# Optimization experiments

Hardware: AMD Instinct MI355X
Metric: run time of the kernel (lower is better)

The kernel has to match this reference:

```python
import jax, jax.numpy as jnp
import numpy as np

B, L, EMBED = 8, 4096, 1024
HEADS, WIN, SHIFT = 16, 128, 64
HD = EMBED // HEADS
MLP_HIDDEN = 4 * EMBED
SCALE = HD ** -0.5
NW = L // WIN


def _layer_norm(x, w, b, eps=1e-5):
    m = x.mean(-1, keepdims=True)
    v = x.var(-1, keepdims=True)
    return (x - m) * jax.lax.rsqrt(v + eps) * w + b


def _compute_mask():
    # replicate SwinBlock1D._compute_mask: region ids over full L, then windowed
    sizes = [L - WIN, WIN - SHIFT, SHIFT]
    region = np.zeros(L, np.int32)
    pos = 0
    for i, s in enumerate(sizes):
        region[pos:pos + s] = i
        pos += s
    region = region.reshape(NW, WIN)
    diff = region[:, None, :] - region[:, :, None]  # (nW, W, W)
    return jnp.asarray(np.where(diff != 0, -100.0, 0.0).astype(np.float32))


_MASK = _compute_mask()
_REL_IDX = jnp.arange(WIN)[None, :] - jnp.arange(WIN)[:, None] + WIN - 1  # (W, W)


def setup_inputs() -> dict:
    key = jax.random.key(0)
    ks = jax.random.split(key, 8)
    s = 0.02

    def w(k, shape):
        return jax.random.normal(k, shape, jnp.float32) * s

    return {
        "x": jax.random.normal(ks[0], (B, L, EMBED), jnp.float32),
        "qkv_w": w(ks[1], (3 * EMBED, EMBED)),
        "qkv_b": jnp.zeros((3 * EMBED,), jnp.float32),
        "proj_w": w(ks[2], (EMBED, EMBED)),
        "proj_b": jnp.zeros((EMBED,), jnp.float32),
        "rpb": w(ks[3], (2 * WIN - 1, HEADS)),
        "norm1_w": jnp.ones((EMBED,), jnp.float32),
        "norm1_b": jnp.zeros((EMBED,), jnp.float32),
        "norm2_w": jnp.ones((EMBED,), jnp.float32),
        "norm2_b": jnp.zeros((EMBED,), jnp.float32),
        "mlp_w1": w(ks[4], (MLP_HIDDEN, EMBED)),
        "mlp_b1": jnp.zeros((MLP_HIDDEN,), jnp.float32),
        "mlp_w2": w(ks[5], (EMBED, MLP_HIDDEN)),
        "mlp_b2": jnp.zeros((EMBED,), jnp.float32),
    }


def reference(x, qkv_w, qkv_b, proj_w, proj_b, rpb,
              norm1_w, norm1_b, norm2_w, norm2_b,
              mlp_w1, mlp_b1, mlp_w2, mlp_b2):
    BW = B * NW
    shortcut = x
    h = _layer_norm(x, norm1_w, norm1_b)
    # shifted-window attention (shift_size > 0)
    h = jnp.roll(h, -SHIFT, axis=1)
    win = h.reshape(BW, WIN, EMBED)
    qkv = (win @ qkv_w.T + qkv_b).reshape(BW, WIN, 3, HEADS, HD)
    qkv = qkv.transpose(2, 0, 3, 1, 4)  # (3, BW, H, W, hd)
    q, k, v = qkv[0], qkv[1], qkv[2]
    attn = jnp.einsum('bhqd,bhkd->bhqk', q, k) * SCALE
    bias = rpb[_REL_IDX]  # (W, W, H)
    attn = attn + bias.transpose(2, 0, 1)[None]
    attn = attn.reshape(B, NW, HEADS, WIN, WIN) + _MASK[None, :, None]
    attn = jax.nn.softmax(attn.reshape(BW, HEADS, WIN, WIN), axis=-1)
    # dropout layers are identity in eval mode
    out = jnp.einsum('bhqk,bhkd->bhqd', attn, v)
    out = out.transpose(0, 2, 1, 3).reshape(BW, WIN, EMBED)
    out = out @ proj_w.T + proj_b
    out = out.reshape(B, L, EMBED)
    out = jnp.roll(out, SHIFT, axis=1)
    x = shortcut + out
    # MLP block
    h2 = _layer_norm(x, norm2_w, norm2_b)
    h2 = jax.nn.gelu(h2 @ mlp_w1.T + mlp_b1, approximate=False) @ mlp_w2.T + mlp_b2
    return x + h2
```

## Files before the change

kernel.cpp:

```cpp
#include <hip/hip_runtime.h>
#include <cstdint>
#include <cstddef>

#define SEQ_L   4096
#define EMBED   1024
#define HEADS   16
#define WINSZ   128
#define SHIFTSZ 64
#define HD      64
#define NWIN    32
#define MTOT    32768
#define ATT_SCALE 0.125f

typedef __bf16 bf16x8 __attribute__((ext_vector_type(8)));
typedef float  f32x4  __attribute__((ext_vector_type(4)));

typedef __attribute__((address_space(3))) void       lds_void;
typedef const __attribute__((address_space(1))) void gbl_void;

#define GLDS16(g, s) __builtin_amdgcn_global_load_lds((gbl_void*)(g), (lds_void*)(s), 16, 0, 0)

__device__ __forceinline__ unsigned short f2bf(float f) {
    unsigned int u = __float_as_uint(f);
    u += 0x7fffu + ((u >> 16) & 1u);
    return (unsigned short)(u >> 16);
}

__launch_bounds__(256)
__global__ void wconv4(const float* __restrict__ s0, const float* __restrict__ s1,
                       const float* __restrict__ s2, const float* __restrict__ s3,
                       unsigned short* __restrict__ d0, unsigned short* __restrict__ d1,
                       unsigned short* __restrict__ d2, unsigned short* __restrict__ d3)
{
    const int b = blockIdx.x;
    const float* s; unsigned short* d; int off;
    if (b < 3072)      { s = s0; d = d0; off = b; }
    else if (b < 4096) { s = s1; d = d1; off = b - 3072; }
    else if (b < 8192) { s = s2; d = d2; off = b - 4096; }
    else               { s = s3; d = d3; off = b - 8192; }
    const int i = (off * 256 + threadIdx.x) * 4;
    const float4 v = *(const float4*)(s + i);
    ushort4 o;
    o.x = f2bf(v.x); o.y = f2bf(v.y); o.z = f2bf(v.z); o.w = f2bf(v.w);
    *(ushort4*)(d + i) = o;
}

__launch_bounds__(256)
__global__ void ln_kernel(const float* __restrict__ x, const float* __restrict__ gw,
                          const float* __restrict__ gb, unsigned short* __restrict__ out,
                          int shift)
{
    const int row  = blockIdx.x * 4 + (threadIdx.x >> 6);
    const int lane = threadIdx.x & 63;
    const int b    = row >> 12;
    const int lw   = row & 4095;
    const int src  = (b << 12) | ((lw + shift) & 4095);
    const float* xr = x + (size_t)src * EMBED;

    float4 v[4];
    float s = 0.f, q = 0.f;
#pragma unroll
    for (int j = 0; j < 4; ++j) {
        v[j] = ((const float4*)xr)[lane + j * 64];
        s += v[j].x + v[j].y + v[j].z + v[j].w;
        q += v[j].x * v[j].x + v[j].y * v[j].y + v[j].z * v[j].z + v[j].w * v[j].w;
    }
#pragma unroll
    for (int off = 32; off > 0; off >>= 1) {
        s += __shfl_xor(s, off);
        q += __shfl_xor(q, off);
    }
    const float mean = s * (1.0f / 1024.0f);
    const float rstd = rsqrtf(q * (1.0f / 1024.0f) - mean * mean + 1e-5f);

    unsigned short* orow = out + (size_t)row * EMBED;
#pragma unroll
    for (int j = 0; j < 4; ++j) {
        const float4 w4 = ((const float4*)gw)[lane + j * 64];
        const float4 b4 = ((const float4*)gb)[lane + j * 64];
        ushort4 o;
        o.x = f2bf((v[j].x - mean) * rstd * w4.x + b4.x);
        o.y = f2bf((v[j].y - mean) * rstd * w4.y + b4.y);
        o.z = f2bf((v[j].z - mean) * rstd * w4.z + b4.z);
        o.w = f2bf((v[j].w - mean) * rstd * w4.w + b4.w);
        ((ushort4*)orow)[lane + j * 64] = o;
    }
}


__device__ __forceinline__ void stage_half(const unsigned short* __restrict__ g, int ldk,
                                           char* ldsbase, int tid)
{
    const int r  = tid >> 3;
    const int cg = ((tid & 7) ^ (r & 7)) << 3;
    GLDS16(g + (size_t)r        * ldk + cg, ldsbase + tid * 16);
    GLDS16(g + (size_t)(r + 64) * ldk + cg, ldsbase + 8192 + tid * 16);
}

__device__ __forceinline__ bf16x8 lds_frag(const char* half, int row, int koff)
{
    const int off = koff ^ ((row & 7) << 4);
    return *(const bf16x8*)(half + row * 128 + off);
}

template<int EPI>
__launch_bounds__(512, 2)
__global__ void gemm256(const unsigned short* __restrict__ A, const unsigned short* __restrict__ W,
                        const float* __restrict__ bias, void* __restrict__ outv,
                        const float* __restrict__ resid, int M, int N, int K)
{
    __shared__ __align__(16) char lds[131072];
    const int tid = threadIdx.x;
    const int l   = tid & 63, w = tid >> 6;
    const int wm  = w >> 2, wn = w & 3;
    const int lr  = l & 15, hi = l >> 4;
    const int k0off = hi << 4;
    const int br0   = (wn & 1) << 6;

    int id = blockIdx.x;
    const int nwg = gridDim.x;
    id = (id & 7) * (nwg >> 3) + (id >> 3);
    const int Ntl = N >> 8;
    const int m0  = (id / Ntl) << 8;
    const int n0  = (id % Ntl) << 8;
    const int NT  = K >> 6;

#define HTB(b, ab, h) (lds + ((((b) << 1 | (ab)) << 1 | (h)) << 14))

    stage_half(A + (size_t)m0         * K,      K, HTB(0,0,0), tid);
    stage_half(A + (size_t)(m0 + 128) * K,      K, HTB(0,0,1), tid);
    stage_half(W + (size_t)n0         * K,      K, HTB(0,1,0), tid);
    stage_half(W + (size_t)(n0 + 128) * K,      K, HTB(0,1,1), tid);
    stage_half(W + (size_t)n0         * K + 64, K, HTB(1,1,0), tid);
    stage_half(W + (size_t)(n0 + 128) * K + 64, K, HTB(1,1,1), tid);
    asm volatile("s_waitcnt vmcnt(4)" ::: "memory");
    __builtin_amdgcn_s_barrier();

    f32x4 acc[8][4];
#pragma unroll
    for (int f = 0; f < 8; ++f)
#pragma unroll
        for (int n = 0; n < 4; ++n)
            acc[f][n] = (f32x4){0.f, 0.f, 0.f, 0.f};

    bf16x8 bf[4][2], af0[2][2], af1[2][2];

#define LOAD_A_BANK(bank, AHP, F0)                                          \
    af##bank[0][0] = lds_frag(AHP, (F0) * 16 + lr,      k0off);             \
    af##bank[0][1] = lds_frag(AHP, (F0) * 16 + lr,      64 + k0off);        \
    af##bank[1][0] = lds_frag(AHP, (F0) * 16 + 16 + lr, k0off);             \
    af##bank[1][1] = lds_frag(AHP, (F0) * 16 + 16 + lr, 64 + k0off);

#define MFMA_BANK(bank, F0)                                                 \
    __builtin_amdgcn_s_setprio(1);                                          \
    _Pragma("unroll")                                                       \
    for (int n = 0; n < 4; ++n) {                                           \
        acc[F0][n]       = __builtin_amdgcn_mfma_f32_16x16x32_bf16(af##bank[0][0], bf[n][0], acc[F0][n], 0, 0, 0);       \
        acc[F0][n]       = __builtin_amdgcn_mfma_f32_16x16x32_bf16(af##bank[0][1], bf[n][1], acc[F0][n], 0, 0, 0);       \
        acc[(F0) + 1][n] = __builtin_amdgcn_mfma_f32_16x16x32_bf16(af##bank[1][0], bf[n][0], acc[(F0) + 1][n], 0, 0, 0); \
        acc[(F0) + 1][n] = __builtin_amdgcn_mfma_f32_16x16x32_bf16(af##bank[1][1], bf[n][1], acc[(F0) + 1][n], 0, 0, 0); \
    }                                                                       \
    __builtin_amdgcn_s_setprio(0);

    {
        const char* Bh0 = HTB(0, 1, wn >> 1);
#pragma unroll
        for (int n = 0; n < 4; ++n) {
            bf[n][0] = lds_frag(Bh0, br0 + n * 16 + lr, k0off);
            bf[n][1] = lds_frag(Bh0, br0 + n * 16 + lr, 64 + k0off);
        }
        const char* Ah0 = HTB(0, 0, wm);
        LOAD_A_BANK(0, Ah0, 0)
    }

#define TILE(BUF)                                                              \
    {                                                                          \
        const char* Ah = HTB(BUF, 0, wm);                                      \
        const unsigned short* An = A + (size_t)m0 * K + (size_t)(t + 1) * 64;  \
        const unsigned short* Wn = W + (size_t)n0 * K + (size_t)(t + 2) * 64;  \
                                    \
        LOAD_A_BANK(1, Ah, 2)                                                  \
        if (t + 1 < NT) {                                                      \
            stage_half(An,                  K, HTB(BUF ^ 1, 0, 0), tid);       \
            stage_half(An + (size_t)128 * K, K, HTB(BUF ^ 1, 0, 1), tid);      \
        }                                                                      \
        asm volatile("s_waitcnt lgkmcnt(4)" ::: "memory");                     \
        MFMA_BANK(0, 0)                                                        \
        __builtin_amdgcn_s_barrier();                                          \
                             \
        LOAD_A_BANK(0, Ah, 4)                                                  \
        if (t + 2 < NT) stage_half(Wn, K, HTB(BUF, 1, 0), tid);                \
        asm volatile("s_waitcnt lgkmcnt(4)" ::: "memory");                     \
        MFMA_BANK(1, 2)                                                        \
           \
        LOAD_A_BANK(1, Ah, 6)                                                  \
        if (t + 2 < NT) stage_half(Wn + (size_t)128 * K, K, HTB(BUF, 1, 1), tid); \
        if (t + 2 < NT) { asm volatile("s_waitcnt vmcnt(4)" ::: "memory"); }   \
        else            { asm volatile("s_waitcnt vmcnt(0)" ::: "memory"); }   \
        asm volatile("s_waitcnt lgkmcnt(4)" ::: "memory");                     \
        MFMA_BANK(0, 4)                                                        \
        __builtin_amdgcn_s_barrier();                                          \
                    \
        if (t + 1 < NT) { const char* AhN = HTB(BUF ^ 1, 0, wm); LOAD_A_BANK(0, AhN, 0) } \
        if (t + 1 < NT) { asm volatile("s_waitcnt lgkmcnt(4)" ::: "memory"); } \
        else            { asm volatile("s_waitcnt lgkmcnt(0)" ::: "memory"); } \
        MFMA_BANK(1, 6)                                                        \
        if (t + 1 < NT) {                                                      \
            const char* BhN = HTB(BUF ^ 1, 1, wn >> 1);                        \
            _Pragma("unroll")                                                  \
            for (int n = 0; n < 4; ++n) {                                      \
                bf[n][0] = lds_frag(BhN, br0 + n * 16 + lr, k0off);            \
                bf[n][1] = lds_frag(BhN, br0 + n * 16 + lr, 64 + k0off);       \
            }                                                                  \
        }                                                                      \
        __builtin_amdgcn_s_barrier();                                          \
    }

    int t;
    for (int u = 0; u < (NT >> 1); ++u) {
        t = 2 * u;     TILE(0)
        t = 2 * u + 1; TILE(1)
    }
#undef TILE
#undef LOAD_A_BANK
#undef MFMA_BANK
#undef HTB

    const int cb = n0 + wn * 64;
    float bv[4];
#pragma unroll
    for (int n = 0; n < 4; ++n) bv[n] = bias[cb + n * 16 + lr];

#pragma unroll
    for (int f = 0; f < 8; ++f) {
        const int mbase = m0 + wm * 128 + f * 16 + hi * 4;
#pragma unroll
        for (int n = 0; n < 4; ++n) {
            const int col = cb + n * 16 + lr;
#pragma unroll
            for (int r = 0; r < 4; ++r) {
                const int m = mbase + r;
                float v = acc[f][n][r] + bv[n];
                if constexpr (EPI == 0) {
                    ((unsigned short*)outv)[(size_t)m * N + col] = f2bf(v);
                } else if constexpr (EPI == 1) {
                    const int bb = m >> 12;
                    const int lw = m & 4095;
                    const int ll = (lw + SHIFTSZ) & 4095;
                    const size_t di = ((size_t)(bb << 12) + ll) * (size_t)N + col;
                    ((float*)outv)[di] = resid[di] + v;
                } else if constexpr (EPI == 2) {
                    const float g = 0.5f * v * (1.0f + erff(v * 0.70710678118654752f));
                    ((unsigned short*)outv)[(size_t)m * N + col] = f2bf(g);
                } else {
                    float* o = (float*)outv;
                    const size_t di = (size_t)m * N + col;
                    o[di] = o[di] + v;
                }
            }
        }
    }
}

#define SM_VT  34816
#define SM_RPB 52224

__device__ __forceinline__ bf16x8 vt_frag(const char* vt, int d, int kbyte)
{
    const int key = ((d >> 3) & 7) << 4;
    return *(const bf16x8*)(vt + d * 272 + (kbyte ^ key));
}

__launch_bounds__(256, 3)
__global__ void attn_kernel(const unsigned short* __restrict__ qkv, const float* __restrict__ rpb,
                            unsigned short* __restrict__ outp)
{
    __shared__ __align__(16) char smem[53248];

    const int t   = threadIdx.x;
    const int l   = t & 63;
    const int w   = t >> 6;
    const int lr  = l & 15;
    const int lq  = l >> 4;
    const int lk  = lq * 8;
    const int blk = blockIdx.x;
    const int win = blk >> 4;
    const int h   = blk & 15;
    const bool masked = ((win & (NWIN - 1)) == NWIN - 1);

    const unsigned short* qb = qkv + (size_t)(win * WINSZ) * (3 * EMBED) + h * HD;
    const unsigned short* kb = qb + EMBED;
    const unsigned short* vb = qb + 2 * EMBED;
    const int mrow = w * 32;
    float* rpbl = (float*)(smem + SM_RPB);

    bf16x8 aqr[2][2];
#pragma unroll
    for (int ks = 0; ks < 2; ++ks)
#pragma unroll
        for (int mi = 0; mi < 2; ++mi)
            aqr[ks][mi] = *(const bf16x8*)(qb + (size_t)(mrow + mi * 16 + lr) * (3 * EMBED) + ks * 32 + lk);

    if (t < 255) rpbl[t] = rpb[t * HEADS + h];

    {
        const int c = t & 7;
#pragma unroll
        for (int p = 0; p < 4; ++p) {
            const int r  = (t >> 3) + p * 32;
            const int cg = (c ^ (r & 7)) << 3;
            GLDS16(kb + (size_t)r * (3 * EMBED) + cg, smem + p * 4096 + t * 16);
        }
    }
    {
        const int c = t & 7;
#pragma unroll
        for (int p = 0; p < 4; ++p) {
            const int k = (t >> 3) + p * 32;
            const uint4 v = *(const uint4*)(vb + (size_t)k * (3 * EMBED) + c * 8);
            const unsigned int vals[4] = {v.x, v.y, v.z, v.w};
            char* base = smem + SM_VT;
#pragma unroll
            for (int e2 = 0; e2 < 4; ++e2) {
                const int d0 = c * 8 + e2 * 2;
                const int key = c << 4;
                *(unsigned short*)(base + d0 * 272 + ((2 * k) ^ key))       = (unsigned short)(vals[e2] & 0xffff);
                *(unsigned short*)(base + (d0 + 1) * 272 + ((2 * k) ^ key)) = (unsigned short)(vals[e2] >> 16);
            }
        }
    }
    asm volatile("s_waitcnt vmcnt(0)" ::: "memory");
    __syncthreads();

    f32x4 sacc[2][8];
#pragma unroll
    for (int a = 0; a < 2; ++a)
#pragma unroll
        for (int b = 0; b < 8; ++b)
            sacc[a][b] = (f32x4){0.f, 0.f, 0.f, 0.f};

#pragma unroll
    for (int ks = 0; ks < 2; ++ks) {
        const int kby = ks * 64 + lq * 16;
        bf16x8 bk8[8];
#pragma unroll
        for (int ni = 0; ni < 8; ++ni)
            bk8[ni] = lds_frag(smem, ni * 16 + lr, kby);
#pragma unroll
        for (int mi = 0; mi < 2; ++mi)
#pragma unroll
            for (int ni = 0; ni < 8; ++ni)
                sacc[mi][ni] = __builtin_amdgcn_mfma_f32_16x16x32_bf16(aqr[ks][mi], bk8[ni], sacc[mi][ni], 0, 0, 0);
    }

    __syncthreads();

#pragma unroll
    for (int mi = 0; mi < 2; ++mi)
#pragma unroll
        for (int r = 0; r < 4; ++r) {
            const int i = mrow + mi * 16 + lq * 4 + r;
            float v[8];
            float mx = -1e30f;
#pragma unroll
            for (int ni = 0; ni < 8; ++ni) {
                const int j = ni * 16 + lr;
                float sv = sacc[mi][ni][r] * ATT_SCALE + rpbl[j - i + WINSZ - 1];
                if (masked && ((i >= SHIFTSZ) != (j >= SHIFTSZ))) sv -= 100.0f;
                v[ni] = sv;
                mx = fmaxf(mx, sv);
            }
#pragma unroll
            for (int s = 1; s < 16; s <<= 1) mx = fmaxf(mx, __shfl_xor(mx, s));
            float sm = 0.f;
#pragma unroll
            for (int ni = 0; ni < 8; ++ni) {
                const float p = __expf(v[ni] - mx);
                v[ni] = p;
                sm += p;
            }
#pragma unroll
            for (int s = 1; s < 16; s <<= 1) sm += __shfl_xor(sm, s);
            const float rs = 1.0f / sm;
#pragma unroll
            for (int ni = 0; ni < 8; ++ni)
                *(unsigned short*)(smem + ((size_t)i * 136 + ni * 16 + lr) * 2) = f2bf(v[ni] * rs);
        }

    __syncthreads();

    f32x4 oacc[2][4];
#pragma unroll
    for (int a = 0; a < 2; ++a)
#pragma unroll
        for (int b = 0; b < 4; ++b)
            oacc[a][b] = (f32x4){0.f, 0.f, 0.f, 0.f};

#pragma unroll
    for (int ks = 0; ks < 4; ++ks) {
        const int k0 = ks * 32;
        bf16x8 ap[2], av[4];
#pragma unroll
        for (int mi = 0; mi < 2; ++mi)
            ap[mi] = *(const bf16x8*)(smem + ((size_t)(mrow + mi * 16 + lr) * 136 + k0 + lk) * 2);
#pragma unroll
        for (int ni = 0; ni < 4; ++ni)
            av[ni] = vt_frag(smem + SM_VT, ni * 16 + lr, k0 * 2 + lq * 16);
#pragma unroll
        for (int mi = 0; mi < 2; ++mi)
#pragma unroll
            for (int ni = 0; ni < 4; ++ni)
                oacc[mi][ni] = __builtin_amdgcn_mfma_f32_16x16x32_bf16(ap[mi], av[ni], oacc[mi][ni], 0, 0, 0);
    }

    unsigned short* ob = outp + (size_t)(win * WINSZ) * EMBED + h * HD;
#pragma unroll
    for (int mi = 0; mi < 2; ++mi)
#pragma unroll
        for (int ni = 0; ni < 4; ++ni)
#pragma unroll
            for (int r = 0; r < 4; ++r) {
                const int i = mrow + mi * 16 + lq * 4 + r;
                const int d = ni * 16 + lr;
                ob[(size_t)i * EMBED + d] = f2bf(oacc[mi][ni][r]);
            }
}

extern "C" void kernel_launch(void* const* d_in, const int* in_sizes, int n_in,
                              void* d_out, int out_size, void* d_ws, size_t ws_size,
                              hipStream_t stream)
{
    const float* x      = (const float*)d_in[0];
    const float* qkv_w  = (const float*)d_in[1];
    const float* qkv_b  = (const float*)d_in[2];
    const float* proj_w = (const float*)d_in[3];
    const float* proj_b = (const float*)d_in[4];
    const float* rpb    = (const float*)d_in[5];
    const float* n1w    = (const float*)d_in[6];
    const float* n1b    = (const float*)d_in[7];
    const float* n2w    = (const float*)d_in[8];
    const float* n2b    = (const float*)d_in[9];
    const float* w1     = (const float*)d_in[10];
    const float* b1     = (const float*)d_in[11];
    const float* w2     = (const float*)d_in[12];
    const float* b2     = (const float*)d_in[13];
    float* out = (float*)d_out;

    unsigned short* wqkv  = (unsigned short*)d_ws;
    unsigned short* wproj = wqkv  + (size_t)3072 * 1024;
    unsigned short* wm1   = wproj + (size_t)1024 * 1024;
    unsigned short* wm2   = wm1   + (size_t)4096 * 1024;
    unsigned short* bufA  = wm2   + (size_t)4096 * 1024;
    unsigned short* bufB  = bufA  + (size_t)MTOT * EMBED;

    wconv4<<<12288, 256, 0, stream>>>(qkv_w, proj_w, w1, w2, wqkv, wproj, wm1, wm2);

    ln_kernel<<<8192, 256, 0, stream>>>(x, n1w, n1b, bufA, SHIFTSZ);

    gemm256<0><<<dim3(1536), 512, 0, stream>>>(bufA, wqkv, qkv_b, bufB, nullptr, MTOT, 3 * EMBED, EMBED);

    attn_kernel<<<4096, 256, 0, stream>>>(bufB, rpb, bufA);

    gemm256<1><<<dim3(512), 512, 0, stream>>>(bufA, wproj, proj_b, out, x, MTOT, EMBED, EMBED);

    ln_kernel<<<8192, 256, 0, stream>>>(out, n2w, n2b, bufA, 0);

    for (int c = 0; c < 2; ++c) {
        const size_t r0 = (size_t)c * 16384;
        gemm256<2><<<dim3(1024), 512, 0, stream>>>(bufA + r0 * EMBED, wm1, b1, bufB, nullptr,
                                                   16384, 4 * EMBED, EMBED);
        gemm256<3><<<dim3(256), 512, 0, stream>>>(bufB, wm2, b2, out + r0 * EMBED, nullptr,
                                                  16384, EMBED, 4 * EMBED);
    }
}
```

Baseline: 1.137 ms.

## Simplify GEMM mainloop to plain double-buffered prefetch with one barrier per tile

```diff
diff --git a/kernel.cpp b/kernel.cpp
--- a/kernel.cpp
+++ b/kernel.cpp
@@ -127,13 +127,11 @@
 
 #define HTB(b, ab, h) (lds + ((((b) << 1 | (ab)) << 1 | (h)) << 14))
 
-    stage_half(A + (size_t)m0         * K,      K, HTB(0,0,0), tid);
-    stage_half(A + (size_t)(m0 + 128) * K,      K, HTB(0,0,1), tid);
-    stage_half(W + (size_t)n0         * K,      K, HTB(0,1,0), tid);
-    stage_half(W + (size_t)(n0 + 128) * K,      K, HTB(0,1,1), tid);
-    stage_half(W + (size_t)n0         * K + 64, K, HTB(1,1,0), tid);
-    stage_half(W + (size_t)(n0 + 128) * K + 64, K, HTB(1,1,1), tid);
-    asm volatile("s_waitcnt vmcnt(4)" ::: "memory");
+    stage_half(A + (size_t)m0         * K, K, HTB(0,0,0), tid);
+    stage_half(A + (size_t)(m0 + 128) * K, K, HTB(0,0,1), tid);
+    stage_half(W + (size_t)n0         * K, K, HTB(0,1,0), tid);
+    stage_half(W + (size_t)(n0 + 128) * K, K, HTB(0,1,1), tid);
+    asm volatile("s_waitcnt vmcnt(0)" ::: "memory");
     __builtin_amdgcn_s_barrier();
 
     f32x4 acc[8][4];
@@ -162,57 +160,38 @@
     }                                                                       \
     __builtin_amdgcn_s_setprio(0);
 
-    {
-        const char* Bh0 = HTB(0, 1, wn >> 1);
-#pragma unroll
-        for (int n = 0; n < 4; ++n) {
-            bf[n][0] = lds_frag(Bh0, br0 + n * 16 + lr, k0off);
-            bf[n][1] = lds_frag(Bh0, br0 + n * 16 + lr, 64 + k0off);
-        }
-        const char* Ah0 = HTB(0, 0, wm);
-        LOAD_A_BANK(0, Ah0, 0)
-    }
-
 #define TILE(BUF)                                                              \
     {                                                                          \
         const char* Ah = HTB(BUF, 0, wm);                                      \
-        const unsigned short* An = A + (size_t)m0 * K + (size_t)(t + 1) * 64;  \
-        const unsigned short* Wn = W + (size_t)n0 * K + (size_t)(t + 2) * 64;  \
-                                    \
+        const char* Bh = HTB(BUF, 1, wn >> 1);                                 \
+                                                        \
+        _Pragma("unroll")                                                      \
+        for (int n = 0; n < 4; ++n) {                                          \
+            bf[n][0] = lds_frag(Bh, br0 + n * 16 + lr, k0off);                 \
+            bf[n][1] = lds_frag(Bh, br0 + n * 16 + lr, 64 + k0off);            \
+        }                                                                      \
+        LOAD_A_BANK(0, Ah, 0)                                                  \
+                                           \
+        if (t + 1 < NT) {                                                      \
+            const unsigned short* An = A + (size_t)m0 * K + (size_t)(t + 1) * 64; \
+            const unsigned short* Wn = W + (size_t)n0 * K + (size_t)(t + 1) * 64; \
+            stage_half(An,                   K, HTB(BUF ^ 1, 0, 0), tid);      \
+            stage_half(An + (size_t)128 * K, K, HTB(BUF ^ 1, 0, 1), tid);      \
+            stage_half(Wn,                   K, HTB(BUF ^ 1, 1, 0), tid);      \
+            stage_half(Wn + (size_t)128 * K, K, HTB(BUF ^ 1, 1, 1), tid);      \
+        }                                                                      \
         LOAD_A_BANK(1, Ah, 2)                                                  \
-        if (t + 1 < NT) {                                                      \
-            stage_half(An,                  K, HTB(BUF ^ 1, 0, 0), tid);       \
-            stage_half(An + (size_t)128 * K, K, HTB(BUF ^ 1, 0, 1), tid);      \
-        }                                                                      \
         asm volatile("s_waitcnt lgkmcnt(4)" ::: "memory");                     \
         MFMA_BANK(0, 0)                                                        \
-        __builtin_amdgcn_s_barrier();                                          \
-                             \
         LOAD_A_BANK(0, Ah, 4)                                                  \
-        if (t + 2 < NT) stage_half(Wn, K, HTB(BUF, 1, 0), tid);                \
         asm volatile("s_waitcnt lgkmcnt(4)" ::: "memory");                     \
         MFMA_BANK(1, 2)                                                        \
-           \
         LOAD_A_BANK(1, Ah, 6)                                                  \
-        if (t + 2 < NT) stage_half(Wn + (size_t)128 * K, K, HTB(BUF, 1, 1), tid); \
-        if (t + 2 < NT) { asm volatile("s_waitcnt vmcnt(4)" ::: "memory"); }   \
-        else            { asm volatile("s_waitcnt vmcnt(0)" ::: "memory"); }   \
         asm volatile("s_waitcnt lgkmcnt(4)" ::: "memory");                     \
         MFMA_BANK(0, 4)                                                        \
-        __builtin_amdgcn_s_barrier();                                          \
-                    \
-        if (t + 1 < NT) { const char* AhN = HTB(BUF ^ 1, 0, wm); LOAD_A_BANK(0, AhN, 0) } \
-        if (t + 1 < NT) { asm volatile("s_waitcnt lgkmcnt(4)" ::: "memory"); } \
-        else            { asm volatile("s_waitcnt lgkmcnt(0)" ::: "memory"); } \
+        asm volatile("s_waitcnt lgkmcnt(0)" ::: "memory");                     \
         MFMA_BANK(1, 6)                                                        \
-        if (t + 1 < NT) {                                                      \
-            const char* BhN = HTB(BUF ^ 1, 1, wn >> 1);                        \
-            _Pragma("unroll")                                                  \
-            for (int n = 0; n < 4; ++n) {                                      \
-                bf[n][0] = lds_frag(BhN, br0 + n * 16 + lr, k0off);            \
-                bf[n][1] = lds_frag(BhN, br0 + n * 16 + lr, 64 + k0off);       \
-            }                                                                  \
-        }                                                                      \
+        asm volatile("s_waitcnt vmcnt(0)" ::: "memory");                       \
         __builtin_amdgcn_s_barrier();                                          \
     }
 
```

Result: no change. 1.137 ms (-0.0%).
